# Performance work log

Measured on AMD Instinct MI355X. Metric: run time of the kernel, lower is better.

The kernel has to match this reference:

```python
import jax, jax.numpy as jnp
import numpy as np

DIM = 1024
HEADS = 16
DIM_HEAD = 64
INNER = HEADS * DIM_HEAD  # 1024
EPS = 1e-5


def layernorm(x, w, b):
    mu = jnp.mean(x, axis=-1, keepdims=True)
    var = jnp.mean(jnp.square(x - mu), axis=-1, keepdims=True)
    return (x - mu) * jax.lax.rsqrt(var + EPS) * w + b


def setup_inputs() -> dict:
    key = jax.random.key(0)
    ks = jax.random.split(key, 9)
    b, n1, n2 = 4, 4096, 256
    x = jax.random.normal(ks[0], (b, n1, DIM), dtype=jnp.float32)
    latents = jax.random.normal(ks[1], (b, n2, DIM), dtype=jnp.float32)
    shift = jax.random.normal(ks[2], (b, HEADS), dtype=jnp.float32)
    scale = jax.random.normal(ks[3], (b, HEADS), dtype=jnp.float32)
    s = 1.0 / np.sqrt(DIM)
    Wq = jax.random.normal(ks[4], (DIM, INNER), dtype=jnp.float32) * s
    Wkv = jax.random.normal(ks[5], (DIM, 2 * INNER), dtype=jnp.float32) * s
    Wout = jax.random.normal(ks[6], (INNER, DIM), dtype=jnp.float32) * (1.0 / np.sqrt(INNER))
    ln1_w = jnp.ones((DIM,), jnp.float32)
    ln1_b = jnp.zeros((DIM,), jnp.float32)
    ln2_w = jnp.ones((DIM,), jnp.float32)
    ln2_b = jnp.zeros((DIM,), jnp.float32)
    return {"x": x, "latents": latents, "shift": shift, "scale": scale,
            "ln1_w": ln1_w, "ln1_b": ln1_b, "ln2_w": ln2_w, "ln2_b": ln2_b,
            "Wq": Wq, "Wkv": Wkv, "Wout": Wout}


def reference(x, latents, shift, scale, ln1_w, ln1_b, ln2_w, ln2_b, Wq, Wkv, Wout):
    b = x.shape[0]
    xn = layernorm(x, ln1_w, ln1_b)            # (b, n1, D)
    ln = layernorm(latents, ln2_w, ln2_b)      # (b, n2, D)
    q = ln @ Wq                                 # (b, n2, inner)
    kv = xn @ Wkv                               # (b, n1, 2*inner)
    k, v = jnp.split(kv, 2, axis=-1)
    q = q.reshape(b, -1, HEADS, DIM_HEAD)
    k = k.reshape(b, -1, HEADS, DIM_HEAD)
    v = v.reshape(b, -1, HEADS, DIM_HEAD)
    # AdaLN-style per-head modulation on q
    q = q * (1.0 + scale[:, None, :, None]) + shift[:, None, :, None]
    # fp32 attention scores (already fp32 here)
    attn_scale = DIM_HEAD ** -0.5
    qk = jnp.einsum('bihd,bjhd->bhij', q.astype(jnp.float32), k.astype(jnp.float32)) * attn_scale
    attn = jax.nn.softmax(qk, axis=-1).astype(v.dtype)  # (b, h, n2, n1)
    out = jnp.einsum('bhij,bjhd->bihd', attn, v)         # (b, n2, h, dh)
    out = out.reshape(b, -1, INNER)
    return out @ Wout
```

## Files before the change

### kernel.cpp

```cpp
#include <hip/hip_runtime.h>

typedef __bf16 bf16;
typedef bf16 bf16x8 __attribute__((ext_vector_type(8)));
typedef bf16 bf16x4 __attribute__((ext_vector_type(4)));
typedef float f32x4 __attribute__((ext_vector_type(4)));

#define B_ 4
#define N1 4096
#define N2 256
#define DIM 1024
#define HEADS 16
#define DH 64
#define INNER 1024
#define ASPLIT 4
#define KEYS_PER_SPLIT (N1 / ASPLIT)
#define SPLIT_ELEMS (4 * 16 * 256 * 64)

typedef __attribute__((address_space(1))) const void gvoid_t;
typedef __attribute__((address_space(3))) void lvoid_t;
__device__ __forceinline__ void async16(const void* g, void* l) {
  __builtin_amdgcn_global_load_lds((gvoid_t*)g, (lvoid_t*)l, 16, 0, 0);
}

__global__ __launch_bounds__(256) void ln_kernel(const float* __restrict__ src,
                                                 const float* __restrict__ w,
                                                 const float* __restrict__ bb,
                                                 bf16* __restrict__ dst) {
  int wv = threadIdx.x >> 6, lane = threadIdx.x & 63;
  int row = blockIdx.x * 4 + wv;
  const float4* p = (const float4*)(src + (size_t)row * DIM);
  float4 v[4];
  for (int j = 0; j < 4; j++) v[j] = p[j * 64 + lane];
  float s = 0.f, sq = 0.f;
  for (int j = 0; j < 4; j++) {
    s += v[j].x + v[j].y + v[j].z + v[j].w;
    sq += v[j].x * v[j].x + v[j].y * v[j].y + v[j].z * v[j].z + v[j].w * v[j].w;
  }
  for (int off = 32; off; off >>= 1) {
    s += __shfl_xor(s, off, 64);
    sq += __shfl_xor(sq, off, 64);
  }
  float mu = s * (1.0f / DIM);
  float var = sq * (1.0f / DIM) - mu * mu;
  float r = rsqrtf(var + 1e-5f);
  for (int j = 0; j < 4; j++) {
    float4 wv4 = ((const float4*)w)[j * 64 + lane];
    float4 bv4 = ((const float4*)bb)[j * 64 + lane];
    bf16x4 o;
    o[0] = (bf16)((v[j].x - mu) * r * wv4.x + bv4.x);
    o[1] = (bf16)((v[j].y - mu) * r * wv4.y + bv4.y);
    o[2] = (bf16)((v[j].z - mu) * r * wv4.z + bv4.z);
    o[3] = (bf16)((v[j].w - mu) * r * wv4.w + bv4.w);
    *(bf16x4*)(dst + (size_t)row * DIM + (j * 64 + lane) * 4) = o;
  }
}

__global__ __launch_bounds__(256) void transpose_w_all(
    const float* __restrict__ Wq, const float* __restrict__ Wkv,
    const float* __restrict__ Wout, bf16* __restrict__ WqT,
    bf16* __restrict__ WkvT, bf16* __restrict__ WoutT) {
  __shared__ float tile[32][33];
  int t = blockIdx.x;
  const float* src;
  bf16* dst;
  int N;
  if (t < 1024) { src = Wq; dst = WqT; N = 1024; }
  else if (t < 3072) { t -= 1024; src = Wkv; dst = WkvT; N = 2048; }
  else { t -= 3072; src = Wout; dst = WoutT; N = 1024; }
  int ntiles = N >> 5;
  int n0 = (t % ntiles) * 32, k0 = (t / ntiles) * 32;
  int x = threadIdx.x, y = threadIdx.y;
  for (int j = 0; j < 4; j++)
    tile[y + 8 * j][x] = src[(size_t)(k0 + y + 8 * j) * N + n0 + x];
  __syncthreads();
  for (int j = 0; j < 4; j++)
    dst[(size_t)(n0 + y + 8 * j) * 1024 + k0 + x] = (bf16)tile[x][y + 8 * j];
}

template <int MODE>
__global__ __launch_bounds__(256) void gemm_bf16(
    const bf16* __restrict__ A, const bf16* __restrict__ Bt,
    void* __restrict__ Cout, void* __restrict__ Cout2, int M, int N, int K,
    const float* __restrict__ shiftp, const float* __restrict__ scalep) {
  __shared__ __align__(16) bf16 smem[128 * 64 * 2];
  bf16* As = smem;
  bf16* Bs = smem + 128 * 64;
  int tid = threadIdx.x;
  int lane = tid & 63, wv = tid >> 6;
  int wr = wv >> 1, wc = wv & 1;
  int quad = lane >> 4, lr = lane & 15;
  int m0 = blockIdx.y * 128, n0 = blockIdx.x * 128;
  f32x4 acc[4][4] = {};
  for (int kt = 0; kt < K; kt += 64) {
    __syncthreads();
    for (int j = 0; j < 4; j++) {
      int idx0 = j * 256 + wv * 64;
      int row = (idx0 >> 3) + (lane >> 3);
      int cb = (lane & 7) ^ (row & 7);
      async16(&A[(size_t)(m0 + row) * K + kt + cb * 8], &As[idx0 * 8]);
      async16(&Bt[(size_t)(n0 + row) * K + kt + cb * 8], &Bs[idx0 * 8]);
    }
    __syncthreads();
    for (int kk = 0; kk < 2; kk++) {
      bf16x8 af[4], bfr[4];
      for (int im = 0; im < 4; im++) {
        int row = wr * 64 + im * 16 + lr;
        af[im] = *(const bf16x8*)&As[row * 64 + ((quad + 4 * kk) ^ (row & 7)) * 8];
      }
      for (int in = 0; in < 4; in++) {
        int row = wc * 64 + in * 16 + lr;
        bfr[in] = *(const bf16x8*)&Bs[row * 64 + ((quad + 4 * kk) ^ (row & 7)) * 8];
      }
      for (int im = 0; im < 4; im++)
        for (int in = 0; in < 4; in++)
          acc[im][in] = __builtin_amdgcn_mfma_f32_16x16x32_bf16(
              af[im], bfr[in], acc[im][in], 0, 0, 0);
    }
  }

  if (MODE == 0 && n0 >= 1024) {
    bf16* Ct = smem;
    for (int pass = 0; pass < 2; pass++) {
      __syncthreads();
      for (int inL = 0; inL < 2; inL++) {
        int in = pass * 2 + inL;
        int cc = wc * 32 + inL * 16 + lr;
        for (int im = 0; im < 4; im++) {
          int rb = wr * 64 + im * 16 + quad * 4;
          bf16x4 pk;
          for (int r = 0; r < 4; r++) pk[r] = (bf16)acc[im][in][r];
          *(bf16x4*)&Ct[cc * 136 + rb] = pk;
        }
      }
      __syncthreads();
      for (int k2 = 0; k2 < 4; k2++) {
        int ci = k2 * 256 + tid;
        int cc = ci >> 4, ch = ci & 15;
        uint4 val = *(const uint4*)&Ct[cc * 136 + ch * 8];
        int gco = (cc >> 5) * 64 + pass * 32 + (cc & 31);
        int col = n0 - 1024 + gco;
        int bb2 = m0 >> 12;
        int key = (m0 & 4095) + ch * 8;
        *(uint4*)&((bf16*)Cout2)[((size_t)(bb2 * 1024 + col)) * 4096 + key] = val;
      }
    }
    return;
  }

  for (int im = 0; im < 4; im++)
    for (int in = 0; in < 4; in++) {
      int col = n0 + wc * 64 + in * 16 + lr;
      for (int r = 0; r < 4; r++) {
        int row = m0 + wr * 64 + im * 16 + quad * 4 + r;
        float v = acc[im][in][r];
        if (MODE == 0) {
          ((bf16*)Cout)[(size_t)row * 1024 + col] = (bf16)v;
        } else if (MODE == 1) {
          int bb = row >> 8, hh = col >> 6;
          float sc = scalep[bb * 16 + hh], sh = shiftp[bb * 16 + hh];
          ((bf16*)Cout)[(size_t)row * N + col] =
              (bf16)((v * (1.0f + sc) + sh) * 0.18033688011112042f);
        } else {
          ((float*)Cout)[(size_t)row * N + col] = v;
        }
      }
    }
}

__global__ __launch_bounds__(256) void attn_kernel(const bf16* __restrict__ q,
                                                   const bf16* __restrict__ kb,
                                                   const bf16* __restrict__ vt,
                                                   float* __restrict__ opA,
                                                   float* __restrict__ opB,
                                                   float* __restrict__ ml) {
  int b = blockIdx.z, h = blockIdx.y;
  int qt = blockIdx.x & 3, sp = blockIdx.x >> 2;
  int tid = threadIdx.x, lane = tid & 63, wv = tid >> 6;
  int quad = lane >> 4, lr = lane & 15;
  __shared__ __align__(16) bf16 Ks[64 * 64];
  __shared__ __align__(16) bf16 Vs[64 * 64];
  __shared__ __align__(16) bf16 QP[64 * 64];
  __shared__ float abuf[4][16];
  int q0 = qt * 64;

  const bf16* qg = q + (size_t)(b * N2 + q0) * INNER + h * DH;
  for (int j = 0; j < 2; j++) {
    int r0 = j * 32 + wv * 8;
    int r = r0 + (lane >> 3);
    async16(&qg[(size_t)r * INNER + ((lane & 7) ^ (r & 7)) * 8], &QP[r0 * 64]);
  }
  __syncthreads();
  bf16x8 aQ[2];
  {
    int row = wv * 16 + lr;
    for (int kk = 0; kk < 2; kk++)
      aQ[kk] = *(const bf16x8*)&QP[row * 64 + ((quad + 4 * kk) ^ (row & 7)) * 8];
  }
  float m_s = -1e30f, l_s = 0.0f;
  f32x4 oacc[4] = {};

  const bf16* kg = kb + (size_t)(b * N1) * 1024 + h * DH;
  const bf16* vg = vt + (size_t)((b * HEADS + h) * DH) * N1;
  bf16* Ps = QP + wv * 1024;

  for (int t = 0; t < KEYS_PER_SPLIT / 64; t++) {
    int key0 = sp * KEYS_PER_SPLIT + t * 64;
    __syncthreads();
    for (int j = 0; j < 2; j++) {
      int r0 = j * 32 + wv * 8;
      int r = r0 + (lane >> 3);
      int cs = ((lane & 7) ^ (r & 7)) * 8;
      async16(&kg[(size_t)(key0 + r) * 1024 + cs], &Ks[r0 * 64]);
      async16(&vg[(size_t)r * N1 + key0 + cs], &Vs[r0 * 64]);
    }
    __syncthreads();

    f32x4 s[4] = {};
    for (int kk = 0; kk < 2; kk++)
      for (int nt = 0; nt < 4; nt++) {
        int row = nt * 16 + lr;
        bf16x8 ak =
            *(const bf16x8*)&Ks[row * 64 + ((quad + 4 * kk) ^ (row & 7)) * 8];
        s[nt] = __builtin_amdgcn_mfma_f32_16x16x32_bf16(ak, aQ[kk], s[nt], 0, 0, 0);
      }

    float mx = s[0][0];
    for (int nt = 0; nt < 4; nt++)
      for (int r = 0; r < 4; r++) mx = fmaxf(mx, s[nt][r]);
    mx = fmaxf(mx, __shfl_xor(mx, 16, 64));
    mx = fmaxf(mx, __shfl_xor(mx, 32, 64));
    float mn = fmaxf(m_s, mx);
    float al = exp2f(m_s - mn);
    float p[4][4], sum = 0.0f;
    for (int nt = 0; nt < 4; nt++)
      for (int r = 0; r < 4; r++) {
        p[nt][r] = exp2f(s[nt][r] - mn);
        sum += p[nt][r];
      }
    sum += __shfl_xor(sum, 16, 64);
    sum += __shfl_xor(sum, 32, 64);
    l_s = l_s * al + sum;
    m_s = mn;
    if (quad == 0) abuf[wv][lr] = al;

    for (int nt = 0; nt < 4; nt++) {
      bf16x4 pk;
      for (int r = 0; r < 4; r++) pk[r] = (bf16)p[nt][r];
      *(bf16x4*)&Ps[lr * 64 + ((2 * nt + (quad >> 1)) ^ (lr & 7)) * 8 +
                    (quad & 1) * 4] = pk;
    }

    f32x4 a4 = *(const f32x4*)&abuf[wv][quad * 4];
    for (int in = 0; in < 4; in++)
      for (int r = 0; r < 4; r++) oacc[in][r] *= a4[r];

    bf16x8 aP[2];
    for (int kk = 0; kk < 2; kk++)
      aP[kk] = *(const bf16x8*)&Ps[lr * 64 + ((4 * kk + quad) ^ (lr & 7)) * 8];

    for (int kk = 0; kk < 2; kk++)
      for (int in = 0; in < 4; in++) {
        int row = in * 16 + lr;
        bf16x8 bv =
            *(const bf16x8*)&Vs[row * 64 + ((quad + 4 * kk) ^ (row & 7)) * 8];
        oacc[in] = __builtin_amdgcn_mfma_f32_16x16x32_bf16(aP[kk], bv, oacc[in], 0, 0, 0);
      }
  }

  float* ob = (sp < 2 ? opA : opB) + (size_t)(sp & 1) * SPLIT_ELEMS;
  size_t rbase = (size_t)(b * HEADS + h) * N2;
  for (int r = 0; r < 4; r++) {
    int qq = q0 + wv * 16 + quad * 4 + r;
    for (int in = 0; in < 4; in++)
      ob[(rbase + qq) * 64 + in * 16 + lr] = oacc[in][r];
  }
  if (quad == 0) {
    int qq = q0 + wv * 16 + lr;
    float* mlp = ml + ((size_t)sp * (4 * HEADS * N2) + rbase + qq) * 2;
    mlp[0] = m_s;
    mlp[1] = l_s;
  }
}

__global__ __launch_bounds__(256) void combine_kernel(const float* __restrict__ opA,
                                                      const float* __restrict__ opB,
                                                      const float* __restrict__ ml,
                                                      bf16* __restrict__ out) {
  int gid = blockIdx.x * 256 + threadIdx.x;
  int d = gid & 63;
  int rq = gid >> 6;
  int qq = rq & 255, bh = rq >> 8;
  int h = bh & 15, b = bh >> 4;
  float m[ASPLIT], l[ASPLIT];
  for (int s = 0; s < ASPLIT; s++) {
    const float* p = ml + ((size_t)s * (4 * HEADS * N2) + rq) * 2;
    m[s] = p[0];
    l[s] = p[1];
  }
  float M = fmaxf(fmaxf(m[0], m[1]), fmaxf(m[2], m[3]));
  float L = 0.0f, o = 0.0f;
  for (int s = 0; s < ASPLIT; s++) {
    float w = exp2f(m[s] - M);
    L += w * l[s];
    const float* op = (s < 2 ? opA : opB) + (size_t)(s & 1) * SPLIT_ELEMS;
    o += w * op[(size_t)rq * 64 + d];
  }
  out[((size_t)(b * N2 + qq)) * INNER + h * DH + d] = (bf16)(o / L);
}

extern "C" void kernel_launch(void* const* d_in, const int* in_sizes, int n_in,
                              void* d_out, int out_size, void* d_ws,
                              size_t ws_size, hipStream_t stream) {
  const float* x       = (const float*)d_in[0];
  const float* latents = (const float*)d_in[1];
  const float* shift   = (const float*)d_in[2];
  const float* scale   = (const float*)d_in[3];
  const float* ln1w    = (const float*)d_in[4];
  const float* ln1b    = (const float*)d_in[5];
  const float* ln2w    = (const float*)d_in[6];
  const float* ln2b    = (const float*)d_in[7];
  const float* Wq      = (const float*)d_in[8];
  const float* Wkv     = (const float*)d_in[9];
  const float* Wout    = (const float*)d_in[10];

  char* ws = (char*)d_ws;
  bf16*  xn    = (bf16*)(ws);
  float* opA   = (float*)(ws);
  bf16*  lnl   = (bf16*)(ws + 33554432);
  float* ml    = (float*)(ws + 33554432);
  bf16*  qb    = (bf16*)(ws + 35651584);
  bf16*  kb    = (bf16*)(ws + 37748736);
  float* opB   = (float*)(ws + 71303168);
  bf16*  vtb   = (bf16*)(ws + 104857600);
  bf16*  aob   = (bf16*)(ws + 138412032);
  bf16*  WqT   = (bf16*)(ws + 140509184);
  bf16*  WkvT  = (bf16*)(ws + 142606336);
  bf16*  WoutT = (bf16*)(ws + 146800640);

  transpose_w_all<<<4096, dim3(32, 8), 0, stream>>>(Wq, Wkv, Wout, WqT, WkvT,
                                                    WoutT);
  ln_kernel<<<4096, 256, 0, stream>>>(x, ln1w, ln1b, xn);
  ln_kernel<<<256, 256, 0, stream>>>(latents, ln2w, ln2b, lnl);

  gemm_bf16<0><<<dim3(16, 128), 256, 0, stream>>>(xn, WkvT, kb, vtb, 16384,
                                                  2048, 1024, nullptr, nullptr);
  gemm_bf16<1><<<dim3(8, 8), 256, 0, stream>>>(lnl, WqT, qb, nullptr, 1024,
                                               1024, 1024, shift, scale);
  attn_kernel<<<dim3(4 * ASPLIT, 16, 4), 256, 0, stream>>>(qb, kb, vtb, opA,
                                                           opB, ml);
  combine_kernel<<<16384, 256, 0, stream>>>(opA, opB, ml, aob);
  gemm_bf16<2><<<dim3(8, 8), 256, 0, stream>>>(aob, WoutT, d_out, nullptr,
                                               1024, 1024, 1024, nullptr, nullptr);
}
```

Baseline: 311.2 us.

## Reuse K/V tiles across four query groups per block and double-buffer loads

The attention kernel now assigns all 256 queries of a head/split to one block, each wave handling 64 queries in four groups, so each K/V tile loaded into LDS is reused four times instead of once. K/V loads are double-buffered with explicit vmcnt waits and raw barriers to overlap the next tile's transfer with compute. The KV-projection GEMM gets a grouped block-index swizzle for better L2 locality. The attention grid shrinks fourfold and register pressure rises, which can reduce occupancy and parallelism.

Result: slower. 326.6 us (+5.0%).

```diff
diff --git a/kernel.cpp b/kernel.cpp
--- a/kernel.cpp
+++ b/kernel.cpp
@@ -21,6 +21,10 @@
 __device__ __forceinline__ void async16(const void* g, void* l) {
   __builtin_amdgcn_global_load_lds((gvoid_t*)g, (lvoid_t*)l, 16, 0, 0);
 }
+
+#define WAIT_VMCNT_4() asm volatile("s_waitcnt vmcnt(4)" ::: "memory")
+#define WAIT_VMCNT_0() asm volatile("s_waitcnt vmcnt(0)" ::: "memory")
+#define HW_BARRIER() asm volatile("s_barrier" ::: "memory")
 
 __global__ __launch_bounds__(256) void ln_kernel(const float* __restrict__ src,
                                                  const float* __restrict__ w,
@@ -89,7 +93,17 @@
   int lane = tid & 63, wv = tid >> 6;
   int wr = wv >> 1, wc = wv & 1;
   int quad = lane >> 4, lr = lane & 15;
-  int m0 = blockIdx.y * 128, n0 = blockIdx.x * 128;
+  int m0, n0;
+  if (MODE == 0) {
+    int bid = blockIdx.y * 16 + blockIdx.x;
+    int c = bid & 7, g = bid >> 3;
+    int mi = g & 7, nb = (g >> 3) & 15, chunk = g >> 7;
+    m0 = (chunk * 64 + mi * 8 + c) * 128;
+    n0 = nb * 128;
+  } else {
+    m0 = blockIdx.y * 128;
+    n0 = blockIdx.x * 128;
+  }
   f32x4 acc[4][4] = {};
   for (int kt = 0; kt < K; kt += 64) {
     __syncthreads();
@@ -173,113 +187,135 @@
                                                    float* __restrict__ opA,
                                                    float* __restrict__ opB,
                                                    float* __restrict__ ml) {
-  int b = blockIdx.z, h = blockIdx.y;
-  int qt = blockIdx.x & 3, sp = blockIdx.x >> 2;
+  int b = blockIdx.z, h = blockIdx.y, sp = blockIdx.x;
   int tid = threadIdx.x, lane = tid & 63, wv = tid >> 6;
   int quad = lane >> 4, lr = lane & 15;
-  __shared__ __align__(16) bf16 Ks[64 * 64];
-  __shared__ __align__(16) bf16 Vs[64 * 64];
-  __shared__ __align__(16) bf16 QP[64 * 64];
+  __shared__ __align__(16) bf16 KV[2][2][64 * 64];
+  __shared__ __align__(16) bf16 QP[4][64 * 64];
   __shared__ float abuf[4][16];
-  int q0 = qt * 64;
-
-  const bf16* qg = q + (size_t)(b * N2 + q0) * INNER + h * DH;
-  for (int j = 0; j < 2; j++) {
-    int r0 = j * 32 + wv * 8;
-    int r = r0 + (lane >> 3);
-    async16(&qg[(size_t)r * INNER + ((lane & 7) ^ (r & 7)) * 8], &QP[r0 * 64]);
-  }
-  __syncthreads();
-  bf16x8 aQ[2];
-  {
-    int row = wv * 16 + lr;
-    for (int kk = 0; kk < 2; kk++)
-      aQ[kk] = *(const bf16x8*)&QP[row * 64 + ((quad + 4 * kk) ^ (row & 7)) * 8];
-  }
-  float m_s = -1e30f, l_s = 0.0f;
-  f32x4 oacc[4] = {};
 
   const bf16* kg = kb + (size_t)(b * N1) * 1024 + h * DH;
   const bf16* vg = vt + (size_t)((b * HEADS + h) * DH) * N1;
-  bf16* Ps = QP + wv * 1024;
+  bf16* Qw = QP[wv];
+  int srow = lane >> 3, sblk = lane & 7;
+
+  const bf16* qg = q + (size_t)(b * N2 + wv * 64) * INNER + h * DH;
+  for (int j = 0; j < 8; j++) {
+    int r = j * 8 + srow;
+    async16(&qg[(size_t)r * INNER + (sblk ^ (r & 7)) * 8], &Qw[j * 512]);
+  }
+  {
+    int key0 = sp * KEYS_PER_SPLIT;
+    for (int j = 0; j < 2; j++) {
+      int r = wv * 16 + j * 8 + srow;
+      async16(&kg[(size_t)(key0 + r) * 1024 + (sblk ^ (r & 7)) * 8],
+              &KV[0][0][(wv * 16 + j * 8) * 64]);
+      async16(&vg[(size_t)r * N1 + key0 + (sblk ^ (r & 7)) * 8],
+              &KV[0][1][(wv * 16 + j * 8) * 64]);
+    }
+  }
+  WAIT_VMCNT_4();
+  bf16x8 aQ[4][2];
+  for (int g = 0; g < 4; g++) {
+    int row = g * 16 + lr;
+    for (int kk = 0; kk < 2; kk++)
+      aQ[g][kk] = *(const bf16x8*)&Qw[row * 64 + ((quad + 4 * kk) ^ (row & 7)) * 8];
+  }
+  float m_s[4], l_s[4];
+  f32x4 oacc[4][4] = {};
+  for (int g = 0; g < 4; g++) { m_s[g] = -1e30f; l_s[g] = 0.0f; }
 
   for (int t = 0; t < KEYS_PER_SPLIT / 64; t++) {
-    int key0 = sp * KEYS_PER_SPLIT + t * 64;
-    __syncthreads();
-    for (int j = 0; j < 2; j++) {
-      int r0 = j * 32 + wv * 8;
-      int r = r0 + (lane >> 3);
-      int cs = ((lane & 7) ^ (r & 7)) * 8;
-      async16(&kg[(size_t)(key0 + r) * 1024 + cs], &Ks[r0 * 64]);
-      async16(&vg[(size_t)r * N1 + key0 + cs], &Vs[r0 * 64]);
-    }
-    __syncthreads();
-
-    f32x4 s[4] = {};
+    if (t + 1 < KEYS_PER_SPLIT / 64) {
+      int key0 = sp * KEYS_PER_SPLIT + (t + 1) * 64;
+      int d = (t + 1) & 1;
+      for (int j = 0; j < 2; j++) {
+        int r = wv * 16 + j * 8 + srow;
+        async16(&kg[(size_t)(key0 + r) * 1024 + (sblk ^ (r & 7)) * 8],
+                &KV[d][0][(wv * 16 + j * 8) * 64]);
+        async16(&vg[(size_t)r * N1 + key0 + (sblk ^ (r & 7)) * 8],
+                &KV[d][1][(wv * 16 + j * 8) * 64]);
+      }
+      WAIT_VMCNT_4();
+    } else {
+      WAIT_VMCNT_0();
+    }
+    HW_BARRIER();
+
+    const bf16* Ks = KV[t & 1][0];
+    const bf16* Vs = KV[t & 1][1];
+    bf16x8 ak[2][4], bvf[2][4];
     for (int kk = 0; kk < 2; kk++)
       for (int nt = 0; nt < 4; nt++) {
         int row = nt * 16 + lr;
-        bf16x8 ak =
+        ak[kk][nt] =
             *(const bf16x8*)&Ks[row * 64 + ((quad + 4 * kk) ^ (row & 7)) * 8];
-        s[nt] = __builtin_amdgcn_mfma_f32_16x16x32_bf16(ak, aQ[kk], s[nt], 0, 0, 0);
-      }
-
-    float mx = s[0][0];
-    for (int nt = 0; nt < 4; nt++)
-      for (int r = 0; r < 4; r++) mx = fmaxf(mx, s[nt][r]);
-    mx = fmaxf(mx, __shfl_xor(mx, 16, 64));
-    mx = fmaxf(mx, __shfl_xor(mx, 32, 64));
-    float mn = fmaxf(m_s, mx);
-    float al = exp2f(m_s - mn);
-    float p[4][4], sum = 0.0f;
-    for (int nt = 0; nt < 4; nt++)
-      for (int r = 0; r < 4; r++) {
-        p[nt][r] = exp2f(s[nt][r] - mn);
-        sum += p[nt][r];
-      }
-    sum += __shfl_xor(sum, 16, 64);
-    sum += __shfl_xor(sum, 32, 64);
-    l_s = l_s * al + sum;
-    m_s = mn;
-    if (quad == 0) abuf[wv][lr] = al;
-
-    for (int nt = 0; nt < 4; nt++) {
-      bf16x4 pk;
-      for (int r = 0; r < 4; r++) pk[r] = (bf16)p[nt][r];
-      *(bf16x4*)&Ps[lr * 64 + ((2 * nt + (quad >> 1)) ^ (lr & 7)) * 8 +
-                    (quad & 1) * 4] = pk;
-    }
-
-    f32x4 a4 = *(const f32x4*)&abuf[wv][quad * 4];
-    for (int in = 0; in < 4; in++)
-      for (int r = 0; r < 4; r++) oacc[in][r] *= a4[r];
-
-    bf16x8 aP[2];
-    for (int kk = 0; kk < 2; kk++)
-      aP[kk] = *(const bf16x8*)&Ps[lr * 64 + ((4 * kk + quad) ^ (lr & 7)) * 8];
-
-    for (int kk = 0; kk < 2; kk++)
-      for (int in = 0; in < 4; in++) {
-        int row = in * 16 + lr;
-        bf16x8 bv =
+        bvf[kk][nt] =
             *(const bf16x8*)&Vs[row * 64 + ((quad + 4 * kk) ^ (row & 7)) * 8];
-        oacc[in] = __builtin_amdgcn_mfma_f32_16x16x32_bf16(aP[kk], bv, oacc[in], 0, 0, 0);
-      }
+      }
+
+    bf16* Ps = Qw;
+    for (int g = 0; g < 4; g++) {
+      f32x4 s[4] = {};
+      for (int kk = 0; kk < 2; kk++)
+        for (int nt = 0; nt < 4; nt++)
+          s[nt] = __builtin_amdgcn_mfma_f32_16x16x32_bf16(ak[kk][nt], aQ[g][kk],
+                                                          s[nt], 0, 0, 0);
+      float mx = s[0][0];
+      for (int nt = 0; nt < 4; nt++)
+        for (int r = 0; r < 4; r++) mx = fmaxf(mx, s[nt][r]);
+      mx = fmaxf(mx, __shfl_xor(mx, 16, 64));
+      mx = fmaxf(mx, __shfl_xor(mx, 32, 64));
+      float mn = fmaxf(m_s[g], mx);
+      float al = exp2f(m_s[g] - mn);
+      float p[4][4], sum = 0.0f;
+      for (int nt = 0; nt < 4; nt++)
+        for (int r = 0; r < 4; r++) {
+          p[nt][r] = exp2f(s[nt][r] - mn);
+          sum += p[nt][r];
+        }
+      sum += __shfl_xor(sum, 16, 64);
+      sum += __shfl_xor(sum, 32, 64);
+      l_s[g] = l_s[g] * al + sum;
+      m_s[g] = mn;
+      if (quad == 0) abuf[wv][lr] = al;
+
+      for (int nt = 0; nt < 4; nt++) {
+        bf16x4 pk;
+        for (int r = 0; r < 4; r++) pk[r] = (bf16)p[nt][r];
+        *(bf16x4*)&Ps[lr * 64 + ((2 * nt + (quad >> 1)) ^ (lr & 7)) * 8 +
+                      (quad & 1) * 4] = pk;
+      }
+      f32x4 a4 = *(const f32x4*)&abuf[wv][quad * 4];
+      for (int in = 0; in < 4; in++)
+        for (int r = 0; r < 4; r++) oacc[g][in][r] *= a4[r];
+
+      bf16x8 aP[2];
+      for (int kk = 0; kk < 2; kk++)
+        aP[kk] = *(const bf16x8*)&Ps[lr * 64 + ((4 * kk + quad) ^ (lr & 7)) * 8];
+      for (int kk = 0; kk < 2; kk++)
+        for (int in = 0; in < 4; in++)
+          oacc[g][in] = __builtin_amdgcn_mfma_f32_16x16x32_bf16(
+              aP[kk], bvf[kk][in], oacc[g][in], 0, 0, 0);
+    }
+    HW_BARRIER();
   }
 
   float* ob = (sp < 2 ? opA : opB) + (size_t)(sp & 1) * SPLIT_ELEMS;
   size_t rbase = (size_t)(b * HEADS + h) * N2;
-  for (int r = 0; r < 4; r++) {
-    int qq = q0 + wv * 16 + quad * 4 + r;
-    for (int in = 0; in < 4; in++)
-      ob[(rbase + qq) * 64 + in * 16 + lr] = oacc[in][r];
-  }
-  if (quad == 0) {
-    int qq = q0 + wv * 16 + lr;
-    float* mlp = ml + ((size_t)sp * (4 * HEADS * N2) + rbase + qq) * 2;
-    mlp[0] = m_s;
-    mlp[1] = l_s;
-  }
+  for (int g = 0; g < 4; g++)
+    for (int r = 0; r < 4; r++) {
+      int qq = wv * 64 + g * 16 + quad * 4 + r;
+      for (int in = 0; in < 4; in++)
+        ob[(rbase + qq) * 64 + in * 16 + lr] = oacc[g][in][r];
+    }
+  if (quad == 0)
+    for (int g = 0; g < 4; g++) {
+      int qq = wv * 64 + g * 16 + lr;
+      float* mlp = ml + ((size_t)sp * (4 * HEADS * N2) + rbase + qq) * 2;
+      mlp[0] = m_s[g];
+      mlp[1] = l_s[g];
+    }
 }
 
 __global__ __launch_bounds__(256) void combine_kernel(const float* __restrict__ opA,
@@ -346,8 +382,8 @@
                                                   2048, 1024, nullptr, nullptr);
   gemm_bf16<1><<<dim3(8, 8), 256, 0, stream>>>(lnl, WqT, qb, nullptr, 1024,
                                                1024, 1024, shift, scale);
-  attn_kernel<<<dim3(4 * ASPLIT, 16, 4), 256, 0, stream>>>(qb, kb, vtb, opA,
-                                                           opB, ml);
+  attn_kernel<<<dim3(ASPLIT, 16, 4), 256, 0, stream>>>(qb, kb, vtb, opA, opB,
+                                                       ml);
   combine_kernel<<<16384, 256, 0, stream>>>(opA, opB, ml, aob);
   gemm_bf16<2><<<dim3(8, 8), 256, 0, stream>>>(aob, WoutT, d_out, nullptr,
                                                1024, 1024, 1024, nullptr, nullptr);
```
